# Kernel optimization log

Hardware: AMD Instinct MI355X
Metric: run time of the kernel (lower is better)

The kernel has to match this reference:

```python
import jax, jax.numpy as jnp
import numpy as np

TREE_DEPTH = 3
N_LEAVES = 2 ** TREE_DEPTH
TEMPERATURE = 1.0
N_HEADS = 16
SOFTPLUS_SHIFT = 0.5413


def _build_path_indices(n_leaves, tree_depth):
    pi = np.zeros((n_leaves, tree_depth), dtype=np.int32)
    pd = np.zeros((n_leaves, tree_depth), dtype=np.float32)
    for leaf in range(n_leaves):
        node = 0
        for d in range(tree_depth):
            pi[leaf, d] = node
            bit = (leaf >> (tree_depth - 1 - d)) & 1
            pd[leaf, d] = 1.0 - bit
            node = 2 * node + 1 + bit
    return pi, pd

PATH_IDX, PATH_DIR = _build_path_indices(N_LEAVES, TREE_DEPTH)


def setup_inputs() -> dict:
    key = jax.random.key(0)
    ks = jax.random.split(key, 8)
    B, S, D = 4, 1024, 1024
    T, N, L, H = 12, 7, 8, 3
    return {
        "x": jax.random.normal(ks[0], (B, S, D), jnp.float32),
        "decision_weights": jax.random.normal(ks[1], (T, N, D), jnp.float32) * 0.1,
        "decision_biases": jnp.zeros((T, N), jnp.float32),
        "node_temperature_logits": jnp.zeros((T, N), jnp.float32),
        "gate_w": jax.random.normal(ks[2], (D, T), jnp.float32) * (1.0 / np.sqrt(D)),
        "gate_b": jnp.zeros((T,), jnp.float32),
        "leaf_outputs": jax.random.normal(ks[3], (H, T, L, D), jnp.float32) * np.sqrt(2.0 / (L + D)),
        "out_w": jax.random.normal(ks[4], (D, D), jnp.float32) * (1.0 / np.sqrt(D)),
        "out_b": jnp.zeros((D,), jnp.float32),
    }


def _forest_qkv(x, dw, db, ntl, gate_w, gate_b, leaf_out):
    # routing: [B,S,T,n_internal]
    decisions = jnp.einsum('bsd,tnd->bstn', x, dw) + db
    node_temps = TEMPERATURE * jax.nn.softplus(ntl + SOFTPLUS_SHIFT)
    decisions = jax.nn.sigmoid(decisions / node_temps)
    # gather nodes along each root-to-leaf path: [B,S,T,L,depth]
    relevant = decisions[..., PATH_IDX]
    probs_per_level = PATH_DIR * relevant + (1.0 - PATH_DIR) * (1.0 - relevant)
    leaf_probs = jnp.prod(probs_per_level, axis=-1)  # [B,S,T,L]
    weights = jax.nn.softmax(x @ gate_w + gate_b, axis=-1)  # [B,S,T]
    # fused per-tree mix + gate combine (same math as per_tree->outputs)
    qkv = jnp.einsum('bstl,bst,htld->hbsd', leaf_probs, weights, leaf_out)
    return qkv[0], qkv[1], qkv[2]


def reference(x, decision_weights, decision_biases, node_temperature_logits,
              gate_w, gate_b, leaf_outputs, out_w, out_b):
    B, S, D = x.shape
    dh = D // N_HEADS
    q, k, v = _forest_qkv(x, decision_weights, decision_biases,
                          node_temperature_logits, gate_w, gate_b, leaf_outputs)
    q = q.reshape(B, S, N_HEADS, dh)
    k = k.reshape(B, S, N_HEADS, dh)
    v = v.reshape(B, S, N_HEADS, dh)
    scale = 1.0 / np.sqrt(dh)
    scores = jnp.einsum('bqhd,bkhd->bhqk', q, k) * scale
    causal = np.tril(np.ones((S, S), dtype=bool))
    scores = jnp.where(causal, scores, jnp.float32(-1e9))
    attn = jax.nn.softmax(scores, axis=-1)
    ctx = jnp.einsum('bhqk,bkhd->bqhd', attn, v).reshape(B, S, D)
    return ctx @ out_w + out_b
```

## Files before the change

kernel.cpp:

```cpp
#include <hip/hip_runtime.h>
#include <hip/hip_bf16.h>
#include <math.h>

#define TOKS 4096

typedef __attribute__((ext_vector_type(4))) float    f32x4;
typedef __attribute__((ext_vector_type(8))) short    short8;
typedef __attribute__((ext_vector_type(4))) unsigned short ushort4v;
typedef unsigned short ushort;

__device__ __forceinline__ ushort f2b(float f) {
    unsigned int b = __float_as_uint(f);
    b += 0x7fff + ((b >> 16) & 1);
    return (ushort)(b >> 16);
}

__global__ __launch_bounds__(256) void routing_kernel(
    const float* __restrict__ x,
    const float* __restrict__ dw,
    const float* __restrict__ db,
    const float* __restrict__ ntl,
    const float* __restrict__ gate_w,
    const float* __restrict__ gate_b,
    ushort* __restrict__ coeffb)
{
    __shared__ float raw[16][96];
    const int tid  = threadIdx.x;
    const int wave = tid >> 6, lane = tid & 63;
    const int tok0 = blockIdx.x * 16 + wave * 4;

    float xr[4][16];
    #pragma unroll
    for (int tkn = 0; tkn < 4; ++tkn)
        #pragma unroll
        for (int ii = 0; ii < 4; ++ii)
            *(float4*)&xr[tkn][ii*4] =
                *(const float4*)&x[(size_t)(tok0 + tkn)*1024 + ii*256 + lane*4];

    #pragma unroll 2
    for (int o = 0; o < 84; ++o) {
        float a0=0.f,a1=0.f,a2=0.f,a3=0.f;
        #pragma unroll
        for (int ii = 0; ii < 4; ++ii) {
            float4 w4 = *(const float4*)&dw[o*1024 + ii*256 + lane*4];
            a0 += w4.x*xr[0][ii*4+0] + w4.y*xr[0][ii*4+1] + w4.z*xr[0][ii*4+2] + w4.w*xr[0][ii*4+3];
            a1 += w4.x*xr[1][ii*4+0] + w4.y*xr[1][ii*4+1] + w4.z*xr[1][ii*4+2] + w4.w*xr[1][ii*4+3];
            a2 += w4.x*xr[2][ii*4+0] + w4.y*xr[2][ii*4+1] + w4.z*xr[2][ii*4+2] + w4.w*xr[2][ii*4+3];
            a3 += w4.x*xr[3][ii*4+0] + w4.y*xr[3][ii*4+1] + w4.z*xr[3][ii*4+2] + w4.w*xr[3][ii*4+3];
        }
        for (int off = 32; off; off >>= 1) {
            a0 += __shfl_down(a0, off); a1 += __shfl_down(a1, off);
            a2 += __shfl_down(a2, off); a3 += __shfl_down(a3, off);
        }
        if (lane == 0) {
            raw[wave*4+0][o] = a0; raw[wave*4+1][o] = a1;
            raw[wave*4+2][o] = a2; raw[wave*4+3][o] = a3;
        }
    }
    for (int t = 0; t < 12; ++t) {
        float a0=0.f,a1=0.f,a2=0.f,a3=0.f;
        #pragma unroll
        for (int ii = 0; ii < 4; ++ii) {
            #pragma unroll
            for (int j = 0; j < 4; ++j) {
                float w = gate_w[(ii*256 + lane*4 + j)*12 + t];
                a0 += w * xr[0][ii*4+j]; a1 += w * xr[1][ii*4+j];
                a2 += w * xr[2][ii*4+j]; a3 += w * xr[3][ii*4+j];
            }
        }
        for (int off = 32; off; off >>= 1) {
            a0 += __shfl_down(a0, off); a1 += __shfl_down(a1, off);
            a2 += __shfl_down(a2, off); a3 += __shfl_down(a3, off);
        }
        if (lane == 0) {
            raw[wave*4+0][84+t] = a0; raw[wave*4+1][84+t] = a1;
            raw[wave*4+2][84+t] = a2; raw[wave*4+3][84+t] = a3;
        }
    }
    __syncthreads();

    if (tid < 192) {
        const int lt = tid / 12, t = tid - lt*12;
        float dec[7];
        #pragma unroll
        for (int n = 0; n < 7; ++n) {
            float tempv = log1pf(expf(ntl[t*7+n] + 0.5413f));
            float v = (raw[lt][t*7+n] + db[t*7+n]) / tempv;
            dec[n] = 1.f / (1.f + expf(-v));
        }
        float g[12], gmax = -3e38f;
        #pragma unroll
        for (int tt = 0; tt < 12; ++tt) {
            g[tt] = raw[lt][84+tt] + gate_b[tt];
            gmax = fmaxf(gmax, g[tt]);
        }
        float gsum = 0.f;
        #pragma unroll
        for (int tt = 0; tt < 12; ++tt) gsum += expf(g[tt]-gmax);
        const float wgt = expf(g[t]-gmax) / gsum;
        const int tok = blockIdx.x*16 + lt;
        #pragma unroll
        for (int l = 0; l < 8; ++l) {
            float p = wgt; int node = 0;
            #pragma unroll
            for (int dpt = 0; dpt < 3; ++dpt) {
                int bit = (l >> (2-dpt)) & 1;
                float r = dec[node];
                p *= bit ? (1.f - r) : r;
                node = 2*node + 1 + bit;
            }
            coeffb[tok*96 + t*8 + l] = f2b(p);
        }
    }
}

__global__ __launch_bounds__(256) void lt_kernel(
    const float* __restrict__ leaf, ushort* __restrict__ leafT)
{
    __shared__ float t[96][65];
    const int d0 = blockIdx.x * 64, h = blockIdx.y;
    const int tid = threadIdx.x;
    for (int i = tid; i < 96*16; i += 256) {
        int k = i >> 4, c4 = i & 15;
        *(float4*)&t[k][c4*4] = *(const float4*)&leaf[(size_t)(h*96 + k)*1024 + d0 + c4*4];
    }
    __syncthreads();
    const int d = tid >> 2, kq = (tid & 3) * 24;
    #pragma unroll
    for (int base = 0; base < 24; base += 8) {
        short8 o;
        #pragma unroll
        for (int j = 0; j < 8; ++j) o[j] = (short)f2b(t[kq+base+j][d]);
        *(short8*)&leafT[(size_t)(h*1024 + d0 + d)*96 + kq + base] = o;
    }
}

__global__ __launch_bounds__(256) void mix_kernel(
    const ushort* __restrict__ coeffb,
    const ushort* __restrict__ leafT,
    ushort* __restrict__ qkvb,
    ushort* __restrict__ vT)
{
    const int bt = blockIdx.x;
    const int bd = blockIdx.y;
    const int tid = threadIdx.x, w = tid >> 6, lane = tid & 63;
    const int lq = lane & 15, lg = lane >> 4;
    const int tok0 = bt*64 + w*16;
    const int c0 = bd*128;
    const int pl = c0 >> 10;
    const int d0 = c0 & 1023;

    f32x4 acc[8];
    #pragma unroll
    for (int n = 0; n < 8; ++n) acc[n] = (f32x4){0.f,0.f,0.f,0.f};

    #pragma unroll
    for (int ks = 0; ks < 3; ++ks) {
        const int k0 = ks*32;
        short8 bfrag = *(const short8*)&coeffb[(tok0 + lq)*96 + k0 + lg*8];
        #pragma unroll
        for (int n = 0; n < 8; ++n) {
            short8 afrag = *(const short8*)&leafT[(size_t)(pl*1024 + d0 + n*16 + lq)*96 + k0 + lg*8];
            acc[n] = __builtin_amdgcn_mfma_f32_16x16x32_bf16(afrag, bfrag, acc[n], 0, 0, 0);
        }
    }

    const int tok = tok0 + lq;
    if (pl < 2) {
        #pragma unroll
        for (int n = 0; n < 8; ++n) {
            const int d = d0 + n*16 + lg*4;
            ushort4v u;
            u[0]=f2b(acc[n][0]); u[1]=f2b(acc[n][1]);
            u[2]=f2b(acc[n][2]); u[3]=f2b(acc[n][3]);
            *(ushort4v*)&qkvb[(size_t)pl*TOKS*1024 + (size_t)tok*1024 + d] = u;
        }
    } else {
        const int b = tok >> 10, seq = tok & 1023;
        #pragma unroll
        for (int n = 0; n < 8; ++n) {
            #pragma unroll
            for (int r = 0; r < 4; ++r) {
                const int d = d0 + n*16 + lg*4 + r;
                const int head = d >> 6, dh = d & 63;
                vT[((size_t)((b*16+head)*64 + dh))*1024 + seq] = f2b(acc[n][r]);
            }
        }
    }
}

__global__ __launch_bounds__(256) void wtrans_kernel(
    const float* __restrict__ w, ushort* __restrict__ wT)
{
    __shared__ float t[64][65];
    const int n0 = blockIdx.x * 64, k0 = blockIdx.y * 64;
    const int tid = threadIdx.x;
    const int r = tid >> 2, c16 = (tid & 3) * 16;
    #pragma unroll
    for (int j = 0; j < 16; j += 4)
        *(float4*)&t[r][c16+j] = *(const float4*)&w[(size_t)(k0+r)*1024 + n0 + c16 + j];
    __syncthreads();
    short8 o0, o1;
    #pragma unroll
    for (int j = 0; j < 8; ++j) o0[j] = (short)f2b(t[c16+j][r]);
    #pragma unroll
    for (int j = 0; j < 8; ++j) o1[j] = (short)f2b(t[c16+8+j][r]);
    *(short8*)&wT[(size_t)(n0+r)*1024 + k0 + c16]     = o0;
    *(short8*)&wT[(size_t)(n0+r)*1024 + k0 + c16 + 8] = o1;
}

__global__ __launch_bounds__(64) void attn_kernel(
    const ushort* __restrict__ qk,
    const ushort* __restrict__ vT,
    ushort* __restrict__ ctxb)
{
    const int id = blockIdx.x;
    const int bh = id & 63;
    const int qt = 63 - (id >> 6);
    const int b = bh >> 4, h = bh & 15;
    const int lane = threadIdx.x;
    const int lq = lane & 15, lg = lane >> 4;
    __shared__ unsigned int pTu[64][13];

    const size_t plane = (size_t)TOKS*1024;
    const int tokq = b*1024 + qt*16 + lq;
    short8 aq[2];
    aq[0] = *(const short8*)&qk[(size_t)tokq*1024 + h*64 + lg*8];
    aq[1] = *(const short8*)&qk[(size_t)tokq*1024 + h*64 + 32 + lg*8];

    f32x4 o[4];
    #pragma unroll
    for (int n = 0; n < 4; ++n) o[n] = (f32x4){0.f,0.f,0.f,0.f};
    float m[4] = {-3e38f,-3e38f,-3e38f,-3e38f};
    float l[4] = {0.f,0.f,0.f,0.f};

    const ushort* Kp  = qk + plane;
    const ushort* vTp = vT + (size_t)bh*64*1024;
    const int nt = (qt >> 2) + 1;

    for (int t = 0; t < nt; ++t) {
        const int tk0 = b*1024 + t*64;
        f32x4 s[4];
        #pragma unroll
        for (int n = 0; n < 4; ++n) s[n] = (f32x4){0.f,0.f,0.f,0.f};
        #pragma unroll
        for (int kk = 0; kk < 2; ++kk)
            #pragma unroll
            for (int n = 0; n < 4; ++n) {
                short8 bk = *(const short8*)&Kp[(size_t)(tk0 + n*16 + lq)*1024 + h*64 + kk*32 + lg*8];
                s[n] = __builtin_amdgcn_mfma_f32_16x16x32_bf16(aq[kk], bk, s[n], 0, 0, 0);
            }

        const bool diag = (t == nt-1);
        if (diag) {
            #pragma unroll
            for (int n = 0; n < 4; ++n)
                #pragma unroll
                for (int r = 0; r < 4; ++r) {
                    float v = s[n][r] * 0.125f;
                    if (t*64 + n*16 + lq > qt*16 + lg*4 + r) v = -1e9f;
                    s[n][r] = v;
                }
        } else {
            #pragma unroll
            for (int n = 0; n < 4; ++n)
                #pragma unroll
                for (int r = 0; r < 4; ++r) s[n][r] *= 0.125f;
        }

        #pragma unroll
        for (int r = 0; r < 4; ++r) {
            float rm = fmaxf(fmaxf(s[0][r], s[1][r]), fmaxf(s[2][r], s[3][r]));
            rm = fmaxf(rm, __shfl_xor(rm, 1));
            rm = fmaxf(rm, __shfl_xor(rm, 2));
            rm = fmaxf(rm, __shfl_xor(rm, 4));
            rm = fmaxf(rm, __shfl_xor(rm, 8));
            float mnew = fmaxf(m[r], rm);
            float corr = __expf(m[r] - mnew);
            float ps = 0.f;
            #pragma unroll
            for (int n = 0; n < 4; ++n) {
                float p = __expf(s[n][r] - mnew);
                s[n][r] = p; ps += p;
            }
            ps += __shfl_xor(ps, 1);
            ps += __shfl_xor(ps, 2);
            ps += __shfl_xor(ps, 4);
            ps += __shfl_xor(ps, 8);
            l[r] = l[r]*corr + ps;
            m[r] = mnew;
            o[0][r] *= corr; o[1][r] *= corr; o[2][r] *= corr; o[3][r] *= corr;
        }

        #pragma unroll
        for (int n = 0; n < 4; ++n) {
            unsigned int lo = (unsigned int)f2b(s[n][0]) | ((unsigned int)f2b(s[n][1]) << 16);
            unsigned int hi = (unsigned int)f2b(s[n][2]) | ((unsigned int)f2b(s[n][3]) << 16);
            pTu[n*16 + lq][lg*2]     = lo;
            pTu[n*16 + lq][lg*2 + 1] = hi;
        }
        __builtin_amdgcn_wave_barrier();

        short8 pa[2];
        #pragma unroll
        for (int kk = 0; kk < 2; ++kk)
            #pragma unroll
            for (int j = 0; j < 8; ++j) {
                unsigned int u = pTu[kk*32 + lg*8 + j][lq >> 1];
                pa[kk][j] = (short)(ushort)(u >> ((lq & 1) * 16));
            }
        __builtin_amdgcn_wave_barrier();

        #pragma unroll
        for (int kk = 0; kk < 2; ++kk)
            #pragma unroll
            for (int n = 0; n < 4; ++n) {
                short8 bv = *(const short8*)&vTp[(size_t)(n*16 + lq)*1024 + t*64 + kk*32 + lg*8];
                o[n] = __builtin_amdgcn_mfma_f32_16x16x32_bf16(pa[kk], bv, o[n], 0, 0, 0);
            }
    }

    #pragma unroll
    for (int r = 0; r < 4; ++r) {
        float inv = 1.f / l[r];
        int row = b*1024 + qt*16 + lg*4 + r;
        #pragma unroll
        for (int n = 0; n < 4; ++n)
            ctxb[(size_t)row*1024 + h*64 + n*16 + lq] = f2b(o[n][r] * inv);
    }
}

__global__ __launch_bounds__(256) void proj_kernel(
    const ushort* __restrict__ A,
    const ushort* __restrict__ Bt,
    const float* __restrict__ bias,
    float* __restrict__ out)
{
    const int bn = blockIdx.x, bm = blockIdx.y;
    const int tid = threadIdx.x, w = tid >> 6, lane = tid & 63;
    const int wm = w >> 1, wn = w & 1;
    const int lq = lane & 15, lg = lane >> 4;
    const int row0 = bm*128 + wm*64;
    const int col0 = bn*128 + wn*64;

    f32x4 acc[4][4];
    #pragma unroll
    for (int i = 0; i < 4; ++i)
        #pragma unroll
        for (int j = 0; j < 4; ++j) acc[i][j] = (f32x4){0.f,0.f,0.f,0.f};

    for (int k0 = 0; k0 < 1024; k0 += 32) {
        short8 a[4], bfr[4];
        #pragma unroll
        for (int i = 0; i < 4; ++i)
            a[i] = *(const short8*)&A[(size_t)(row0 + i*16 + lq)*1024 + k0 + lg*8];
        #pragma unroll
        for (int j = 0; j < 4; ++j)
            bfr[j] = *(const short8*)&Bt[(size_t)(col0 + j*16 + lq)*1024 + k0 + lg*8];
        #pragma unroll
        for (int i = 0; i < 4; ++i)
            #pragma unroll
            for (int j = 0; j < 4; ++j)
                acc[i][j] = __builtin_amdgcn_mfma_f32_16x16x32_bf16(a[i], bfr[j], acc[i][j], 0, 0, 0);
    }

    #pragma unroll
    for (int i = 0; i < 4; ++i)
        #pragma unroll
        for (int j = 0; j < 4; ++j) {
            int col = col0 + j*16 + lq;
            float bb = bias[col];
            #pragma unroll
            for (int r = 0; r < 4; ++r)
                out[(size_t)(row0 + i*16 + lg*4 + r)*1024 + col] = acc[i][j][r] + bb;
        }
}

extern "C" void kernel_launch(void* const* d_in, const int* in_sizes, int n_in,
                              void* d_out, int out_size, void* d_ws, size_t ws_size,
                              hipStream_t stream) {
    (void)in_sizes; (void)n_in; (void)out_size; (void)ws_size;
    const float* x      = (const float*)d_in[0];
    const float* dw     = (const float*)d_in[1];
    const float* db     = (const float*)d_in[2];
    const float* ntl    = (const float*)d_in[3];
    const float* gate_w = (const float*)d_in[4];
    const float* gate_b = (const float*)d_in[5];
    const float* leaf   = (const float*)d_in[6];
    const float* out_w  = (const float*)d_in[7];
    const float* out_b  = (const float*)d_in[8];
    float* out = (float*)d_out;

    ushort* coeffb = (ushort*)d_ws;
    ushort* qkvb   = (ushort*)((char*)d_ws + ((size_t)2u  << 20));
    ushort* vT     = (ushort*)((char*)d_ws + ((size_t)20u << 20));
    ushort* ctxb   = (ushort*)((char*)d_ws + ((size_t)30u << 20));
    ushort* wT     = (ushort*)((char*)d_ws + ((size_t)40u << 20));
    ushort* leafT  = (ushort*)((char*)d_ws + ((size_t)44u << 20));

    hipLaunchKernelGGL(routing_kernel, dim3(256),     dim3(256), 0, stream,
                       x, dw, db, ntl, gate_w, gate_b, coeffb);
    hipLaunchKernelGGL(lt_kernel,      dim3(16, 3),   dim3(256), 0, stream,
                       leaf, leafT);
    hipLaunchKernelGGL(wtrans_kernel,  dim3(16, 16),  dim3(256), 0, stream,
                       out_w, wT);
    hipLaunchKernelGGL(mix_kernel,     dim3(64, 24),  dim3(256), 0, stream,
                       coeffb, leafT, qkvb, vT);
    hipLaunchKernelGGL(attn_kernel,    dim3(4096),    dim3(64),  0, stream,
                       qkvb, vT, ctxb);
    hipLaunchKernelGGL(proj_kernel,    dim3(8, 32),   dim3(256), 0, stream,
                       ctxb, wT, out_b, out);
}
```

Before: 295.6 us.

## Compute routing logits with bf16 MFMA using a pre-converted weight matrix

Replaces the FP32 shuffle-reduction routing GEMV with a new kernel that packs decision and gate weights into one bf16 [96x1024] matrix. A single-wave kernel then computes the logits for 16 tokens with 16x16x32 bf16 MFMA instructions. The aim is to remove the slow scalar FMA and cross-lane reduction work in routing and to write the coefficients with vector stores. In exchange it adds an extra conversion kernel and lowers the precision of the routing logits to bf16 inputs.

```diff
diff --git a/kernel.cpp b/kernel.cpp
--- a/kernel.cpp
+++ b/kernel.cpp
@@ -15,90 +15,86 @@
     return (ushort)(b >> 16);
 }
 
-__global__ __launch_bounds__(256) void routing_kernel(
+__global__ __launch_bounds__(256) void wb_kernel(
+    const float* __restrict__ dw,
+    const float* __restrict__ gate_w,
+    ushort* __restrict__ Wb)
+{
+    const int i = blockIdx.x * 256 + threadIdx.x;
+    const int row = i >> 7, k0 = (i & 127) * 8;
+    short8 o;
+    if (row < 84) {
+        float4 a0 = *(const float4*)&dw[(size_t)row*1024 + k0];
+        float4 a1 = *(const float4*)&dw[(size_t)row*1024 + k0 + 4];
+        o[0]=(short)f2b(a0.x); o[1]=(short)f2b(a0.y); o[2]=(short)f2b(a0.z); o[3]=(short)f2b(a0.w);
+        o[4]=(short)f2b(a1.x); o[5]=(short)f2b(a1.y); o[6]=(short)f2b(a1.z); o[7]=(short)f2b(a1.w);
+    } else {
+        const int t = row - 84;
+        #pragma unroll
+        for (int j = 0; j < 8; ++j) o[j] = (short)f2b(gate_w[(size_t)(k0+j)*12 + t]);
+    }
+    *(short8*)&Wb[(size_t)row*1024 + k0] = o;
+}
+
+__global__ __launch_bounds__(64) void route2_kernel(
     const float* __restrict__ x,
-    const float* __restrict__ dw,
+    const ushort* __restrict__ Wb,
     const float* __restrict__ db,
     const float* __restrict__ ntl,
-    const float* __restrict__ gate_w,
     const float* __restrict__ gate_b,
     ushort* __restrict__ coeffb)
 {
-    __shared__ float raw[16][96];
-    const int tid  = threadIdx.x;
-    const int wave = tid >> 6, lane = tid & 63;
-    const int tok0 = blockIdx.x * 16 + wave * 4;
-
-    float xr[4][16];
-    #pragma unroll
-    for (int tkn = 0; tkn < 4; ++tkn)
-        #pragma unroll
-        for (int ii = 0; ii < 4; ++ii)
-            *(float4*)&xr[tkn][ii*4] =
-                *(const float4*)&x[(size_t)(tok0 + tkn)*1024 + ii*256 + lane*4];
-
-    #pragma unroll 2
-    for (int o = 0; o < 84; ++o) {
-        float a0=0.f,a1=0.f,a2=0.f,a3=0.f;
-        #pragma unroll
-        for (int ii = 0; ii < 4; ++ii) {
-            float4 w4 = *(const float4*)&dw[o*1024 + ii*256 + lane*4];
-            a0 += w4.x*xr[0][ii*4+0] + w4.y*xr[0][ii*4+1] + w4.z*xr[0][ii*4+2] + w4.w*xr[0][ii*4+3];
-            a1 += w4.x*xr[1][ii*4+0] + w4.y*xr[1][ii*4+1] + w4.z*xr[1][ii*4+2] + w4.w*xr[1][ii*4+3];
-            a2 += w4.x*xr[2][ii*4+0] + w4.y*xr[2][ii*4+1] + w4.z*xr[2][ii*4+2] + w4.w*xr[2][ii*4+3];
-            a3 += w4.x*xr[3][ii*4+0] + w4.y*xr[3][ii*4+1] + w4.z*xr[3][ii*4+2] + w4.w*xr[3][ii*4+3];
-        }
-        for (int off = 32; off; off >>= 1) {
-            a0 += __shfl_down(a0, off); a1 += __shfl_down(a1, off);
-            a2 += __shfl_down(a2, off); a3 += __shfl_down(a3, off);
-        }
-        if (lane == 0) {
-            raw[wave*4+0][o] = a0; raw[wave*4+1][o] = a1;
-            raw[wave*4+2][o] = a2; raw[wave*4+3][o] = a3;
-        }
-    }
-    for (int t = 0; t < 12; ++t) {
-        float a0=0.f,a1=0.f,a2=0.f,a3=0.f;
-        #pragma unroll
-        for (int ii = 0; ii < 4; ++ii) {
-            #pragma unroll
-            for (int j = 0; j < 4; ++j) {
-                float w = gate_w[(ii*256 + lane*4 + j)*12 + t];
-                a0 += w * xr[0][ii*4+j]; a1 += w * xr[1][ii*4+j];
-                a2 += w * xr[2][ii*4+j]; a3 += w * xr[3][ii*4+j];
-            }
-        }
-        for (int off = 32; off; off >>= 1) {
-            a0 += __shfl_down(a0, off); a1 += __shfl_down(a1, off);
-            a2 += __shfl_down(a2, off); a3 += __shfl_down(a3, off);
-        }
-        if (lane == 0) {
-            raw[wave*4+0][84+t] = a0; raw[wave*4+1][84+t] = a1;
-            raw[wave*4+2][84+t] = a2; raw[wave*4+3][84+t] = a3;
-        }
-    }
-    __syncthreads();
-
-    if (tid < 192) {
-        const int lt = tid / 12, t = tid - lt*12;
+    const int tok0 = blockIdx.x * 16;
+    const int lane = threadIdx.x;
+    const int lq = lane & 15, lg = lane >> 4;
+    __shared__ float lgt[16][97];
+
+    f32x4 acc[6];
+    #pragma unroll
+    for (int n = 0; n < 6; ++n) acc[n] = (f32x4){0.f,0.f,0.f,0.f};
+
+    for (int k0 = 0; k0 < 1024; k0 += 32) {
+        float4 a0 = *(const float4*)&x[(size_t)(tok0 + lq)*1024 + k0 + lg*8];
+        float4 a1 = *(const float4*)&x[(size_t)(tok0 + lq)*1024 + k0 + lg*8 + 4];
+        short8 af;
+        af[0]=(short)f2b(a0.x); af[1]=(short)f2b(a0.y); af[2]=(short)f2b(a0.z); af[3]=(short)f2b(a0.w);
+        af[4]=(short)f2b(a1.x); af[5]=(short)f2b(a1.y); af[6]=(short)f2b(a1.z); af[7]=(short)f2b(a1.w);
+        #pragma unroll
+        for (int n = 0; n < 6; ++n) {
+            short8 bf_ = *(const short8*)&Wb[(size_t)(n*16 + lq)*1024 + k0 + lg*8];
+            acc[n] = __builtin_amdgcn_mfma_f32_16x16x32_bf16(af, bf_, acc[n], 0, 0, 0);
+        }
+    }
+
+    #pragma unroll
+    for (int n = 0; n < 6; ++n)
+        #pragma unroll
+        for (int r = 0; r < 4; ++r)
+            lgt[lg*4 + r][n*16 + lq] = acc[n][r];
+    __builtin_amdgcn_wave_barrier();
+
+    const int tok = lane >> 2;
+    #pragma unroll
+    for (int tj = 0; tj < 3; ++tj) {
+        const int t = (lane & 3)*3 + tj;
         float dec[7];
         #pragma unroll
         for (int n = 0; n < 7; ++n) {
             float tempv = log1pf(expf(ntl[t*7+n] + 0.5413f));
-            float v = (raw[lt][t*7+n] + db[t*7+n]) / tempv;
+            float v = (lgt[tok][t*7+n] + db[t*7+n]) / tempv;
             dec[n] = 1.f / (1.f + expf(-v));
         }
         float g[12], gmax = -3e38f;
         #pragma unroll
         for (int tt = 0; tt < 12; ++tt) {
-            g[tt] = raw[lt][84+tt] + gate_b[tt];
+            g[tt] = lgt[tok][84+tt] + gate_b[tt];
             gmax = fmaxf(gmax, g[tt]);
         }
         float gsum = 0.f;
         #pragma unroll
         for (int tt = 0; tt < 12; ++tt) gsum += expf(g[tt]-gmax);
         const float wgt = expf(g[t]-gmax) / gsum;
-        const int tok = blockIdx.x*16 + lt;
+        short8 co;
         #pragma unroll
         for (int l = 0; l < 8; ++l) {
             float p = wgt; int node = 0;
@@ -109,8 +105,9 @@
                 p *= bit ? (1.f - r) : r;
                 node = 2*node + 1 + bit;
             }
-            coeffb[tok*96 + t*8 + l] = f2b(p);
-        }
+            co[l] = (short)f2b(p);
+        }
+        *(short8*)&coeffb[(size_t)(tok0 + tok)*96 + t*8] = co;
     }
 }
 
@@ -392,18 +389,21 @@
     float* out = (float*)d_out;
 
     ushort* coeffb = (ushort*)d_ws;
+    ushort* Wb     = (ushort*)((char*)d_ws + ((size_t)1u  << 20));
     ushort* qkvb   = (ushort*)((char*)d_ws + ((size_t)2u  << 20));
     ushort* vT     = (ushort*)((char*)d_ws + ((size_t)20u << 20));
     ushort* ctxb   = (ushort*)((char*)d_ws + ((size_t)30u << 20));
     ushort* wT     = (ushort*)((char*)d_ws + ((size_t)40u << 20));
     ushort* leafT  = (ushort*)((char*)d_ws + ((size_t)44u << 20));
 
-    hipLaunchKernelGGL(routing_kernel, dim3(256),     dim3(256), 0, stream,
-                       x, dw, db, ntl, gate_w, gate_b, coeffb);
+    hipLaunchKernelGGL(wb_kernel,      dim3(48),      dim3(256), 0, stream,
+                       dw, gate_w, Wb);
     hipLaunchKernelGGL(lt_kernel,      dim3(16, 3),   dim3(256), 0, stream,
                        leaf, leafT);
     hipLaunchKernelGGL(wtrans_kernel,  dim3(16, 16),  dim3(256), 0, stream,
                        out_w, wT);
+    hipLaunchKernelGGL(route2_kernel,  dim3(256),     dim3(64),  0, stream,
+                       x, Wb, db, ntl, gate_b, coeffb);
     hipLaunchKernelGGL(mix_kernel,     dim3(64, 24),  dim3(256), 0, stream,
                        coeffb, leafT, qkvb, vT);
     hipLaunchKernelGGL(attn_kernel,    dim3(4096),    dim3(64),  0, stream,
```

New measurement: 275.7 us. 6.7% less time.
